# Performance work log

Measured on AMD Instinct MI355X. Metric: run time of the kernel, lower is better.

The kernel has to match this reference:

```python
import jax, jax.numpy as jnp
import numpy as np

B, D, H = 4096, 64, 1024  # batch, state dim, hidden width


def setup_inputs() -> dict:
    key = jax.random.key(0)
    ks = jax.random.split(key, 4)
    def w(k, shape, fan_in):
        return (jax.random.normal(k, shape, jnp.float32) / np.float32(np.sqrt(fan_in)))
    return {
        "x": jax.random.normal(ks[0], (B, 1 + D), jnp.float32),
        "W1": w(ks[1], (D, H), D),
        "b1": jnp.zeros((H,), jnp.float32),
        "W2": w(ks[2], (H, H), H),
        "b2": jnp.zeros((H,), jnp.float32),
        "W3": w(ks[3], (H, D), H),
        "b3": jnp.zeros((D,), jnp.float32),
    }


def _mlp(z, W1, b1, W2, b2, W3, b3):
    # tanh MLP vector field: d -> h -> h -> d
    h = jnp.tanh(z @ W1 + b1)
    h = jnp.tanh(h @ W2 + b2)
    return h @ W3 + b3


def reference(x, W1, b1, W2, b2, W3, b3):
    x_in = x[:, 1:]                        # [B, D] state (col 0 is logp channel)
    f = lambda z: _mlp(z, W1, b1, W2, b2, W3, b3)
    x_out = f(x_in)                        # [B, D]

    # Exact Jacobian trace: same math as the torch per-dim autograd.grad loop,
    # expressed as D forward-mode JVPs vmapped over the identity basis.
    eye = jnp.eye(x_in.shape[1], dtype=x.dtype)

    def diag_entry(e):                     # e: [D] basis vector
        _, t = jax.jvp(f, (x_in,), (jnp.broadcast_to(e, x_in.shape),))
        return t @ e                       # [B] = J[:, i, i]

    trJ = jnp.sum(jax.vmap(diag_entry)(eye), axis=0)  # [B]

    out = jnp.concatenate([-trJ[:, None], x_out], axis=1)  # [B, 1+D]
    return out + 0.0 * x  # faithful to `+ 0 * x` in the original
```

## Files before the change

kernel.cpp:

```cpp
#include <hip/hip_runtime.h>
#include <cmath>

typedef unsigned short u16;
typedef __attribute__((ext_vector_type(8))) short s8v;
typedef __attribute__((ext_vector_type(4))) float f4v;
typedef __attribute__((ext_vector_type(16))) float f16v;

__device__ __forceinline__ u16 f2bf(float f) {
    union { float f; unsigned u; } v; v.f = f;
    unsigned r = v.u + 0x7FFFu + ((v.u >> 16) & 1u);
    return (u16)(r >> 16);
}
__device__ __forceinline__ float tanh_fast(float x) {
    float e = __builtin_amdgcn_exp2f(x * 2.88539008177792681f);
    return 1.f - 2.f * __builtin_amdgcn_rcpf(1.f + e);
}
__device__ __forceinline__ int wslot(int row, int c) {
    return ((((c >> 2) << 6) | ((c & 3) << 4) | (row & 15)) ^ c);
}
__device__ __forceinline__ size_t fragoff(int n, int k) {
    return (((size_t)(n >> 5) * 64 + (k >> 4)) * 64 + (n & 31) + (((k >> 3) & 1) << 5)) * 8 + (k & 7);
}

__launch_bounds__(256)
__global__ void cnf_prep(const float* __restrict__ x, const float* __restrict__ W1,
                         const float* __restrict__ W2, const float* __restrict__ W3,
                         u16* __restrict__ W2Tf, u16* __restrict__ VTf,
                         u16* __restrict__ xb, u16* __restrict__ W1T,
                         u16* __restrict__ W3Tf, float* __restrict__ trJ)
{
    __shared__ float w2s[32][33];
    __shared__ __align__(16) float w1s[64][36];
    const int a = blockIdx.x * 32;
    const int b = blockIdx.y * 32;
    const int t = threadIdx.x;

    #pragma unroll
    for (int it = 0; it < 4; ++it) {
        int idx = t + it * 256;
        w2s[idx >> 5][idx & 31] = W2[(a + (idx >> 5)) * 1024 + b + (idx & 31)];
    }
    #pragma unroll
    for (int it = 0; it < 8; ++it) {
        int idx = t + it * 256;
        w1s[idx >> 5][idx & 31] = W1[(idx >> 5) * 1024 + a + (idx & 31)];
    }
    __syncthreads();

    #pragma unroll
    for (int it = 0; it < 4; ++it) {
        int idx = t + it * 256;
        int rr = idx >> 5, cc = idx & 31;
        W2Tf[fragoff(b + rr, a + cc)] = f2bf(w2s[cc][rr]);
    }
    {
        const int q = t >> 3, pg = t & 7;
        const float* w3row = W3 + (b + q) * 64;
        f4v u = f4v{0.f, 0.f, 0.f, 0.f};
        #pragma unroll
        for (int i4 = 0; i4 < 16; ++i4) {
            f4v w3v = *(const f4v*)&w3row[i4 * 4];
            #pragma unroll
            for (int s = 0; s < 4; ++s) {
                f4v wv = *(const f4v*)&w1s[i4 * 4 + s][pg * 4];
                u += w3v[s] * wv;
            }
        }
        #pragma unroll
        for (int j = 0; j < 4; ++j) {
            const int pp = pg * 4 + j;
            VTf[fragoff(b + q, a + pp)] = f2bf(w2s[pp][q] * u[j]);
        }
    }
    {
        int bid = blockIdx.y * 32 + blockIdx.x;
        int e = bid * 256 + t;
        xb[e] = f2bf(x[(e >> 6) * 65 + 1 + (e & 63)]);
    }
    if (blockIdx.y == 0) {
        int pp = t >> 3, i0 = (t & 7) * 8;
        s8v v;
        #pragma unroll
        for (int j = 0; j < 8; ++j) v[j] = (short)f2bf(w1s[i0 + j][pp]);
        *(s8v*)&W1T[(a + pp) * 64 + i0] = v;
        if (t < 128) trJ[blockIdx.x * 128 + t] = 0.f;
    }
    if (blockIdx.y == 1) {
        int idx = blockIdx.x * 256 + t;
        int n = idx & 63, k0 = (idx >> 6) * 8;
        s8v v;
        #pragma unroll
        for (int j = 0; j < 8; ++j) v[j] = (short)f2bf(W3[(k0 + j) * 64 + n]);
        *(s8v*)&W3Tf[fragoff(n, k0)] = v;
    }
}

__launch_bounds__(256)
__global__ void cnf_gemm1(const u16* __restrict__ xb, const u16* __restrict__ W1T,
                          const float* __restrict__ b1,
                          u16* __restrict__ h1, u16* __restrict__ g1)
{
    __shared__ __align__(16) u16 lds[12 * 1024];
    __shared__ __align__(16) u16 hls[128 * 64];
    __shared__ __align__(16) u16 gls[128 * 64];
    const int t = threadIdx.x;
    const int wave = t >> 6, lane = t & 63;
    const int wm = wave >> 1, wn = wave & 1;
    const int g = lane >> 4, lr = lane & 15;
    const int arow0 = blockIdx.x * 128, bcol0 = blockIdx.y * 64;

    #pragma unroll
    for (int i = 0; i < 4; ++i) {
        int ch = t + i * 256, row = ch >> 3, c = ch & 7;
        *(s8v*)&lds[(row >> 4) * 1024 + wslot(row, c) * 8] =
            *(const s8v*)&xb[(arow0 + row) * 64 + c * 8];
    }
    #pragma unroll
    for (int i = 0; i < 2; ++i) {
        int ch = t + i * 256, row = ch >> 3, c = ch & 7;
        *(s8v*)&lds[(8 + (row >> 4)) * 1024 + wslot(row, c) * 8] =
            *(const s8v*)&W1T[(bcol0 + row) * 64 + c * 8];
    }
    __syncthreads();

    f4v acc[4][2];
    #pragma unroll
    for (int mi = 0; mi < 4; ++mi)
        #pragma unroll
        for (int ni = 0; ni < 2; ++ni) acc[mi][ni] = f4v{0.f,0.f,0.f,0.f};

    #pragma unroll
    for (int ks = 0; ks < 2; ++ks) {
        const int lo = (ks * 64 + (lane ^ ((ks * 4 + g) & 7))) * 8;
        s8v af[4], bf[2];
        #pragma unroll
        for (int mi = 0; mi < 4; ++mi) af[mi] = *(const s8v*)&lds[(wm * 4 + mi) * 1024 + lo];
        #pragma unroll
        for (int ni = 0; ni < 2; ++ni) bf[ni] = *(const s8v*)&lds[(8 + wn * 2 + ni) * 1024 + lo];
        #pragma unroll
        for (int mi = 0; mi < 4; ++mi)
            #pragma unroll
            for (int ni = 0; ni < 2; ++ni)
                acc[mi][ni] = __builtin_amdgcn_mfma_f32_16x16x32_bf16(af[mi], bf[ni], acc[mi][ni], 0, 0, 0);
    }

    #pragma unroll
    for (int mi = 0; mi < 4; ++mi) {
        const int rowl = wm * 64 + mi * 16 + g * 4;
        #pragma unroll
        for (int ni = 0; ni < 2; ++ni) {
            const int coll = wn * 32 + ni * 16 + lr;
            const float bv = b1[bcol0 + coll];
            const int cc = coll >> 3, jj = coll & 7;
            #pragma unroll
            for (int r = 0; r < 4; ++r) {
                const int row = rowl + r;
                float h = tanh_fast(acc[mi][ni][r] + bv);
                int idx = row * 64 + ((cc ^ (row & 7)) << 3) + jj;
                hls[idx] = f2bf(h);
                gls[idx] = f2bf(1.f - h * h);
            }
        }
    }
    __syncthreads();

    #pragma unroll
    for (int i = 0; i < 4; ++i) {
        int id = i * 256 + t;
        int row = id >> 3, ch = id & 7;
        int src = row * 64 + ((ch ^ (row & 7)) << 3);
        size_t dst = (size_t)(arow0 + row) * 1024 + bcol0 + ch * 8;
        *(s8v*)&h1[dst] = *(const s8v*)&hls[src];
        *(s8v*)&g1[dst] = *(const s8v*)&gls[src];
    }
}

#define LOADA(dh, dg, ko) \
    do { dh = *(const s8v*)(h1p + (ko)); dg = *(const s8v*)(g1p + (ko)); } while (0)

#define LOADB(B, kkg)                                                          \
    do { _Pragma("unroll")                                                     \
         for (int _ks = 0; _ks < 2; ++_ks) {                                   \
             size_t _o = (((size_t)(ntb + wn) * 64 + (kkg) * 2 + _ks) * 64 + lane) * 8; \
             B[_ks*2 + 0] = *(const s8v*)&W2Tf[_o];                            \
             B[_ks*2 + 1] = *(const s8v*)&VTf[_o];                             \
         } } while (0)

#define WRITEA(sh, sg, bb)                                                     \
    do { u16* _wb = &lds[bb][0];                                               \
         *(s8v*)&_wb[sdst] = sh; *(s8v*)&_wb[4096 + sdst] = sg; } while (0)

#define MIDBODY(kt, AwH, AwG, AlH, AlG, Bc, Bn)                                \
    {                                                                          \
        if ((kt) < 30) { const int _ko = ((kt) + 2) * 32; LOADA(AlH, AlG, _ko); } \
        if ((kt) < 31) { WRITEA(AwH, AwG, ((kt) + 1) & 1); LOADB(Bn, (kt) + 1); } \
        const u16* buf = &lds[(kt) & 1][0];                                    \
        _Pragma("unroll")                                                      \
        for (int ks = 0; ks < 2; ++ks) {                                       \
            const int lp = (lane ^ ((lane >> 5) << 2) ^ (ks << 1)) * 8;        \
            s8v a1[2], a2[2];                                                  \
            _Pragma("unroll")                                                  \
            for (int mt = 0; mt < 2; ++mt) {                                   \
                const int R = (wrt * 2 + mt) * 2 + ks;                         \
                a1[mt] = *(const s8v*)&buf[R * 512 + lp];                      \
                a2[mt] = *(const s8v*)&buf[4096 + R * 512 + lp];               \
            }                                                                  \
            _Pragma("unroll")                                                  \
            for (int mt = 0; mt < 2; ++mt) {                                   \
                acc1[mt] = __builtin_amdgcn_mfma_f32_32x32x16_bf16(a1[mt], Bc[ks*2+0], acc1[mt], 0, 0, 0); \
                acc2[mt] = __builtin_amdgcn_mfma_f32_32x32x16_bf16(a2[mt], Bc[ks*2+1], acc2[mt], 0, 0, 0); \
            }                                                                  \
        }                                                                      \
        __syncthreads();                                                       \
    }

__launch_bounds__(512, 1)
__global__ void cnf_mid(const u16* __restrict__ h1, const u16* __restrict__ g1,
                        const u16* __restrict__ W2Tf, const u16* __restrict__ VTf,
                        const float* __restrict__ b2,
                        u16* __restrict__ h2f, float* __restrict__ trJ)
{
    __shared__ __align__(16) u16 lds[2][8192];

    const int t = threadIdx.x;
    const int wave = t >> 6, lane = t & 63;
    const int wrt = wave & 1;
    const int wn  = wave >> 1;
    const int arow0 = blockIdx.x * 128;
    const int ntb = blockIdx.y * 4;

    const int row = t >> 2, c = t & 3;
    const int R0 = (row >> 5) * 2 + (c >> 1);
    const int L0 = (row & 31) + ((c & 1) << 5);
    const int sdst = (R0 * 64 + (L0 ^ ((L0 >> 5) << 2) ^ ((R0 & 1) << 1))) * 8;
    const u16* h1p = h1 + (size_t)(arow0 + row) * 1024 + c * 8;
    const u16* g1p = g1 + (size_t)(arow0 + row) * 1024 + c * 8;

    f16v acc1[2], acc2[2];
    #pragma unroll
    for (int mt = 0; mt < 2; ++mt)
        #pragma unroll
        for (int r = 0; r < 16; ++r) { acc1[mt][r] = 0.f; acc2[mt][r] = 0.f; }

    s8v ahA, agA, ahB, agB;
    s8v bA[4], bB[4];

    LOADA(ahA, agA, 0);
    WRITEA(ahA, agA, 0);
    LOADA(ahB, agB, 32);
    LOADB(bA, 0);
    __syncthreads();

    for (int kt2 = 0; kt2 < 16; ++kt2) {
        const int kt = kt2 * 2;
        MIDBODY(kt,     ahB, agB, ahA, agA, bA, bB);
        MIDBODY(kt + 1, ahA, agA, ahB, agB, bB, bA);
    }

    const int l31 = lane & 31, lh = lane >> 5;
    #pragma unroll
    for (int mt = 0; mt < 2; ++mt) {
        const int rt = (arow0 >> 5) + wrt * 2 + mt;
        const int q0 = (ntb + wn) * 32;
        const float bv = b2[q0 + l31];
        const size_t hb = (((size_t)rt * 64 + ((q0 + l31) >> 4)) * 64
                           + (((l31 >> 3) & 1) << 5)) * 8 + (l31 & 7) + lh * 32;
        float tr[16];
        #pragma unroll
        for (int r = 0; r < 16; ++r) {
            float hh = tanh_fast(acc1[mt][r] + bv);
            float gg = 1.f - hh * hh;
            h2f[hb + ((r & 3) + ((r >> 2) << 3)) * 8] = f2bf(hh);
            tr[r] = acc2[mt][r] * gg;
        }
        #pragma unroll
        for (int off = 1; off < 32; off <<= 1)
            #pragma unroll
            for (int r = 0; r < 16; ++r) tr[r] += __shfl_xor(tr[r], off);
        if (l31 == 0) {
            const int rowb = arow0 + (wrt * 2 + mt) * 32 + lh * 4;
            #pragma unroll
            for (int r = 0; r < 16; ++r)
                atomicAdd(&trJ[rowb + (r & 3) + ((r >> 2) << 3)], tr[r]);
        }
    }
}

__launch_bounds__(256)
__global__ void cnf_out(const u16* __restrict__ h2f, const u16* __restrict__ W3Tf,
                        const float* __restrict__ b3, const float* __restrict__ trJ,
                        float* __restrict__ out)
{
    __shared__ float red[4][32][64];
    const int t = threadIdx.x;
    const int wave = t >> 6, lane = t & 63;
    const int rt = blockIdx.x;

    f16v acc[2];
    #pragma unroll
    for (int ni = 0; ni < 2; ++ni)
        #pragma unroll
        for (int r = 0; r < 16; ++r) acc[ni][r] = 0.f;

    #pragma unroll
    for (int kki = 0; kki < 16; ++kki) {
        const int kk = wave * 16 + kki;
        s8v af = *(const s8v*)&h2f[(((size_t)rt * 64 + kk) * 64 + lane) * 8];
        #pragma unroll
        for (int ni = 0; ni < 2; ++ni) {
            s8v bf = *(const s8v*)&W3Tf[(((size_t)ni * 64 + kk) * 64 + lane) * 8];
            acc[ni] = __builtin_amdgcn_mfma_f32_32x32x16_bf16(af, bf, acc[ni], 0, 0, 0);
        }
    }
    const int l31 = lane & 31, lh = lane >> 5;
    #pragma unroll
    for (int ni = 0; ni < 2; ++ni)
        #pragma unroll
        for (int r = 0; r < 16; ++r)
            red[wave][(r & 3) + ((r >> 2) << 3) + lh * 4][ni * 32 + l31] = acc[ni][r];
    __syncthreads();

    #pragma unroll
    for (int i = 0; i < 8; ++i) {
        int o = t * 8 + i;
        int row = o >> 6, col = o & 63;
        float s = red[0][row][col] + red[1][row][col] + red[2][row][col] + red[3][row][col] + b3[col];
        out[(size_t)(rt * 32 + row) * 65 + 1 + col] = s;
    }
    if (t < 32) out[(size_t)(rt * 32 + t) * 65] = -trJ[rt * 32 + t];
}

extern "C" void kernel_launch(void* const* d_in, const int* in_sizes, int n_in,
                              void* d_out, int out_size, void* d_ws, size_t ws_size,
                              hipStream_t stream) {
    const float* x  = (const float*)d_in[0];
    const float* W1 = (const float*)d_in[1];
    const float* b1 = (const float*)d_in[2];
    const float* W2 = (const float*)d_in[3];
    const float* b2 = (const float*)d_in[4];
    const float* W3 = (const float*)d_in[5];
    const float* b3 = (const float*)d_in[6];
    float* out = (float*)d_out;

    char* ws = (char*)d_ws;
    u16*   h1b = (u16*)(ws);
    u16*   g1b = (u16*)(ws + (size_t)( 8u << 20));
    u16*   h2f = (u16*)(ws + (size_t)(16u << 20));
    u16*   W2T = (u16*)(ws + (size_t)(24u << 20));
    u16*   VTb = (u16*)(ws + (size_t)(26u << 20));
    float* trJ = (float*)(ws + (size_t)(28u << 20));
    u16*   xbb = (u16*)(ws + (size_t)(28u << 20) + 65536);
    u16*   W1T = (u16*)(ws + (size_t)(28u << 20) + 65536 + 524288);
    u16*   W3T = (u16*)(ws + (size_t)(28u << 20) + 65536 + 524288 + 131072);

    cnf_prep <<<dim3(32, 32), 256, 0, stream>>>(x, W1, W2, W3, W2T, VTb, xbb, W1T, W3T, trJ);
    cnf_gemm1<<<dim3(32, 16), 256, 0, stream>>>(xbb, W1T, b1, h1b, g1b);
    cnf_mid  <<<dim3(32, 8),  512, 0, stream>>>(h1b, g1b, W2T, VTb, b2, h2f, trJ);
    cnf_out  <<<128,          256, 0, stream>>>(h2f, W3T, b3, trJ, out);
}
```

Baseline: 55.49 us.

## Merge first-layer GEMM into prep kernel and split output GEMM across column halves

The separate gemm1 kernel is folded into the prep launch as extra blockIdx.y rows. Those blocks convert x and W1 to bf16 fragments directly in shared memory, which removes the xb/W1T intermediate buffers and one kernel launch. The output kernel now splits its 64 output columns across two blocks per row tile, doubling the block count to improve occupancy. The cost is a larger shared-memory arena for every prep block, which may lower occupancy of the weight-prep blocks, and some redundant A-fragment loads in the output kernel.

```diff
diff --git a/kernel.cpp b/kernel.cpp
--- a/kernel.cpp
+++ b/kernel.cpp
@@ -25,153 +25,154 @@
 __launch_bounds__(256)
 __global__ void cnf_prep(const float* __restrict__ x, const float* __restrict__ W1,
                          const float* __restrict__ W2, const float* __restrict__ W3,
+                         const float* __restrict__ b1,
                          u16* __restrict__ W2Tf, u16* __restrict__ VTf,
-                         u16* __restrict__ xb, u16* __restrict__ W1T,
-                         u16* __restrict__ W3Tf, float* __restrict__ trJ)
+                         u16* __restrict__ W3Tf,
+                         u16* __restrict__ h1, u16* __restrict__ g1,
+                         float* __restrict__ trJ)
 {
-    __shared__ float w2s[32][33];
-    __shared__ __align__(16) float w1s[64][36];
-    const int a = blockIdx.x * 32;
-    const int b = blockIdx.y * 32;
+    __shared__ __align__(16) char arena[57344];
     const int t = threadIdx.x;
 
-    #pragma unroll
-    for (int it = 0; it < 4; ++it) {
-        int idx = t + it * 256;
-        w2s[idx >> 5][idx & 31] = W2[(a + (idx >> 5)) * 1024 + b + (idx & 31)];
-    }
-    #pragma unroll
-    for (int it = 0; it < 8; ++it) {
-        int idx = t + it * 256;
-        w1s[idx >> 5][idx & 31] = W1[(idx >> 5) * 1024 + a + (idx & 31)];
-    }
-    __syncthreads();
-
-    #pragma unroll
-    for (int it = 0; it < 4; ++it) {
-        int idx = t + it * 256;
-        int rr = idx >> 5, cc = idx & 31;
-        W2Tf[fragoff(b + rr, a + cc)] = f2bf(w2s[cc][rr]);
-    }
-    {
-        const int q = t >> 3, pg = t & 7;
-        const float* w3row = W3 + (b + q) * 64;
-        f4v u = f4v{0.f, 0.f, 0.f, 0.f};
-        #pragma unroll
-        for (int i4 = 0; i4 < 16; ++i4) {
-            f4v w3v = *(const f4v*)&w3row[i4 * 4];
-            #pragma unroll
-            for (int s = 0; s < 4; ++s) {
-                f4v wv = *(const f4v*)&w1s[i4 * 4 + s][pg * 4];
-                u += w3v[s] * wv;
+    if (blockIdx.y < 32) {
+        float (*w2s)[33] = (float (*)[33])arena;
+        float (*w1s)[36] = (float (*)[36])(arena + 4352);
+        const int a = blockIdx.x * 32;
+        const int b = blockIdx.y * 32;
+
+        #pragma unroll
+        for (int it = 0; it < 4; ++it) {
+            int idx = t + it * 256;
+            w2s[idx >> 5][idx & 31] = W2[(a + (idx >> 5)) * 1024 + b + (idx & 31)];
+        }
+        #pragma unroll
+        for (int it = 0; it < 8; ++it) {
+            int idx = t + it * 256;
+            w1s[idx >> 5][idx & 31] = W1[(idx >> 5) * 1024 + a + (idx & 31)];
+        }
+        __syncthreads();
+
+        #pragma unroll
+        for (int it = 0; it < 4; ++it) {
+            int idx = t + it * 256;
+            int rr = idx >> 5, cc = idx & 31;
+            W2Tf[fragoff(b + rr, a + cc)] = f2bf(w2s[cc][rr]);
+        }
+        {
+            const int q = t >> 3, pg = t & 7;
+            const float* w3row = W3 + (b + q) * 64;
+            f4v u = f4v{0.f, 0.f, 0.f, 0.f};
+            #pragma unroll
+            for (int i4 = 0; i4 < 16; ++i4) {
+                f4v w3v = *(const f4v*)&w3row[i4 * 4];
+                #pragma unroll
+                for (int s = 0; s < 4; ++s) {
+                    f4v wv = *(const f4v*)&w1s[i4 * 4 + s][pg * 4];
+                    u += w3v[s] * wv;
+                }
             }
-        }
-        #pragma unroll
-        for (int j = 0; j < 4; ++j) {
-            const int pp = pg * 4 + j;
-            VTf[fragoff(b + q, a + pp)] = f2bf(w2s[pp][q] * u[j]);
-        }
-    }
-    {
-        int bid = blockIdx.y * 32 + blockIdx.x;
-        int e = bid * 256 + t;
-        xb[e] = f2bf(x[(e >> 6) * 65 + 1 + (e & 63)]);
-    }
-    if (blockIdx.y == 0) {
-        int pp = t >> 3, i0 = (t & 7) * 8;
-        s8v v;
-        #pragma unroll
-        for (int j = 0; j < 8; ++j) v[j] = (short)f2bf(w1s[i0 + j][pp]);
-        *(s8v*)&W1T[(a + pp) * 64 + i0] = v;
-        if (t < 128) trJ[blockIdx.x * 128 + t] = 0.f;
-    }
-    if (blockIdx.y == 1) {
-        int idx = blockIdx.x * 256 + t;
-        int n = idx & 63, k0 = (idx >> 6) * 8;
-        s8v v;
-        #pragma unroll
-        for (int j = 0; j < 8; ++j) v[j] = (short)f2bf(W3[(k0 + j) * 64 + n]);
-        *(s8v*)&W3Tf[fragoff(n, k0)] = v;
-    }
-}
-
-__launch_bounds__(256)
-__global__ void cnf_gemm1(const u16* __restrict__ xb, const u16* __restrict__ W1T,
-                          const float* __restrict__ b1,
-                          u16* __restrict__ h1, u16* __restrict__ g1)
-{
-    __shared__ __align__(16) u16 lds[12 * 1024];
-    __shared__ __align__(16) u16 hls[128 * 64];
-    __shared__ __align__(16) u16 gls[128 * 64];
-    const int t = threadIdx.x;
-    const int wave = t >> 6, lane = t & 63;
-    const int wm = wave >> 1, wn = wave & 1;
-    const int g = lane >> 4, lr = lane & 15;
-    const int arow0 = blockIdx.x * 128, bcol0 = blockIdx.y * 64;
-
-    #pragma unroll
-    for (int i = 0; i < 4; ++i) {
-        int ch = t + i * 256, row = ch >> 3, c = ch & 7;
-        *(s8v*)&lds[(row >> 4) * 1024 + wslot(row, c) * 8] =
-            *(const s8v*)&xb[(arow0 + row) * 64 + c * 8];
-    }
-    #pragma unroll
-    for (int i = 0; i < 2; ++i) {
-        int ch = t + i * 256, row = ch >> 3, c = ch & 7;
-        *(s8v*)&lds[(8 + (row >> 4)) * 1024 + wslot(row, c) * 8] =
-            *(const s8v*)&W1T[(bcol0 + row) * 64 + c * 8];
-    }
-    __syncthreads();
-
-    f4v acc[4][2];
-    #pragma unroll
-    for (int mi = 0; mi < 4; ++mi)
-        #pragma unroll
-        for (int ni = 0; ni < 2; ++ni) acc[mi][ni] = f4v{0.f,0.f,0.f,0.f};
-
-    #pragma unroll
-    for (int ks = 0; ks < 2; ++ks) {
-        const int lo = (ks * 64 + (lane ^ ((ks * 4 + g) & 7))) * 8;
-        s8v af[4], bf[2];
-        #pragma unroll
-        for (int mi = 0; mi < 4; ++mi) af[mi] = *(const s8v*)&lds[(wm * 4 + mi) * 1024 + lo];
-        #pragma unroll
-        for (int ni = 0; ni < 2; ++ni) bf[ni] = *(const s8v*)&lds[(8 + wn * 2 + ni) * 1024 + lo];
+            #pragma unroll
+            for (int j = 0; j < 4; ++j) {
+                const int pp = pg * 4 + j;
+                VTf[fragoff(b + q, a + pp)] = f2bf(w2s[pp][q] * u[j]);
+            }
+        }
+        if (blockIdx.y == 0 && t < 128) trJ[blockIdx.x * 128 + t] = 0.f;
+        if (blockIdx.y == 1) {
+            int idx = blockIdx.x * 256 + t;
+            int n = idx & 63, k0 = (idx >> 6) * 8;
+            s8v v;
+            #pragma unroll
+            for (int j = 0; j < 8; ++j) v[j] = (short)f2bf(W3[(k0 + j) * 64 + n]);
+            *(s8v*)&W3Tf[fragoff(n, k0)] = v;
+        }
+    } else {
+        const int wave = t >> 6, lane = t & 63;
+        const int wm = wave >> 1, wn = wave & 1;
+        const int g = lane >> 4, lr = lane & 15;
+        const int arow0 = blockIdx.x * 128;
+        const int bcol0 = (blockIdx.y - 32) * 64;
+
+        u16*  frg = (u16*)arena;
+        float (*w1f)[65] = (float (*)[65])(arena + 24576);
+        u16*  hls = (u16*)(arena + 24576);
+        u16*  gls = (u16*)(arena + 24576 + 16384);
+
+        #pragma unroll
+        for (int it = 0; it < 16; ++it) {
+            int idx = t + it * 256;
+            int row = idx >> 6, col = idx & 63;
+            w1f[row][col] = W1[row * 1024 + bcol0 + col];
+        }
+        #pragma unroll
+        for (int it = 0; it < 32; ++it) {
+            int e = t + it * 256;
+            int row = e >> 6, col = e & 63;
+            frg[(row >> 4) * 1024 + wslot(row, col >> 3) * 8 + (col & 7)] =
+                f2bf(x[(arow0 + row) * 65 + 1 + col]);
+        }
+        __syncthreads();
+        #pragma unroll
+        for (int it = 0; it < 2; ++it) {
+            int id = t + it * 256;
+            int p = id >> 3, c = id & 7;
+            s8v v;
+            #pragma unroll
+            for (int j = 0; j < 8; ++j) v[j] = (short)f2bf(w1f[c * 8 + j][p]);
+            *(s8v*)&frg[(8 + (p >> 4)) * 1024 + wslot(p, c) * 8] = v;
+        }
+        __syncthreads();
+
+        f4v acc[4][2];
         #pragma unroll
         for (int mi = 0; mi < 4; ++mi)
             #pragma unroll
-            for (int ni = 0; ni < 2; ++ni)
-                acc[mi][ni] = __builtin_amdgcn_mfma_f32_16x16x32_bf16(af[mi], bf[ni], acc[mi][ni], 0, 0, 0);
-    }
-
-    #pragma unroll
-    for (int mi = 0; mi < 4; ++mi) {
-        const int rowl = wm * 64 + mi * 16 + g * 4;
-        #pragma unroll
-        for (int ni = 0; ni < 2; ++ni) {
-            const int coll = wn * 32 + ni * 16 + lr;
-            const float bv = b1[bcol0 + coll];
-            const int cc = coll >> 3, jj = coll & 7;
-            #pragma unroll
-            for (int r = 0; r < 4; ++r) {
-                const int row = rowl + r;
-                float h = tanh_fast(acc[mi][ni][r] + bv);
-                int idx = row * 64 + ((cc ^ (row & 7)) << 3) + jj;
-                hls[idx] = f2bf(h);
-                gls[idx] = f2bf(1.f - h * h);
+            for (int ni = 0; ni < 2; ++ni) acc[mi][ni] = f4v{0.f,0.f,0.f,0.f};
+
+        #pragma unroll
+        for (int ks = 0; ks < 2; ++ks) {
+            const int lo = (ks * 64 + (lane ^ ((ks * 4 + g) & 7))) * 8;
+            s8v af[4], bf[2];
+            #pragma unroll
+            for (int mi = 0; mi < 4; ++mi) af[mi] = *(const s8v*)&frg[(wm * 4 + mi) * 1024 + lo];
+            #pragma unroll
+            for (int ni = 0; ni < 2; ++ni) bf[ni] = *(const s8v*)&frg[(8 + wn * 2 + ni) * 1024 + lo];
+            #pragma unroll
+            for (int mi = 0; mi < 4; ++mi)
+                #pragma unroll
+                for (int ni = 0; ni < 2; ++ni)
+                    acc[mi][ni] = __builtin_amdgcn_mfma_f32_16x16x32_bf16(af[mi], bf[ni], acc[mi][ni], 0, 0, 0);
+        }
+
+        #pragma unroll
+        for (int mi = 0; mi < 4; ++mi) {
+            const int rowl = wm * 64 + mi * 16 + g * 4;
+            #pragma unroll
+            for (int ni = 0; ni < 2; ++ni) {
+                const int coll = wn * 32 + ni * 16 + lr;
+                const float bv = b1[bcol0 + coll];
+                const int cc = coll >> 3, jj = coll & 7;
+                #pragma unroll
+                for (int r = 0; r < 4; ++r) {
+                    const int row = rowl + r;
+                    float h = tanh_fast(acc[mi][ni][r] + bv);
+                    int idx = row * 64 + ((cc ^ (row & 7)) << 3) + jj;
+                    hls[idx] = f2bf(h);
+                    gls[idx] = f2bf(1.f - h * h);
+                }
             }
         }
-    }
-    __syncthreads();
-
-    #pragma unroll
-    for (int i = 0; i < 4; ++i) {
-        int id = i * 256 + t;
-        int row = id >> 3, ch = id & 7;
-        int src = row * 64 + ((ch ^ (row & 7)) << 3);
-        size_t dst = (size_t)(arow0 + row) * 1024 + bcol0 + ch * 8;
-        *(s8v*)&h1[dst] = *(const s8v*)&hls[src];
-        *(s8v*)&g1[dst] = *(const s8v*)&gls[src];
+        __syncthreads();
+
+        #pragma unroll
+        for (int i = 0; i < 4; ++i) {
+            int id = i * 256 + t;
+            int row = id >> 3, ch = id & 7;
+            int src = row * 64 + ((ch ^ (row & 7)) << 3);
+            size_t dst = (size_t)(arow0 + row) * 1024 + bcol0 + ch * 8;
+            *(s8v*)&h1[dst] = *(const s8v*)&hls[src];
+            *(s8v*)&g1[dst] = *(const s8v*)&gls[src];
+        }
     }
 }
 
@@ -291,43 +292,38 @@
                         const float* __restrict__ b3, const float* __restrict__ trJ,
                         float* __restrict__ out)
 {
-    __shared__ float red[4][32][64];
+    __shared__ float red[4][32][32];
     const int t = threadIdx.x;
     const int wave = t >> 6, lane = t & 63;
     const int rt = blockIdx.x;
-
-    f16v acc[2];
-    #pragma unroll
-    for (int ni = 0; ni < 2; ++ni)
-        #pragma unroll
-        for (int r = 0; r < 16; ++r) acc[ni][r] = 0.f;
+    const int nb = blockIdx.y;
+
+    f16v acc;
+    #pragma unroll
+    for (int r = 0; r < 16; ++r) acc[r] = 0.f;
 
     #pragma unroll
     for (int kki = 0; kki < 16; ++kki) {
         const int kk = wave * 16 + kki;
         s8v af = *(const s8v*)&h2f[(((size_t)rt * 64 + kk) * 64 + lane) * 8];
-        #pragma unroll
-        for (int ni = 0; ni < 2; ++ni) {
-            s8v bf = *(const s8v*)&W3Tf[(((size_t)ni * 64 + kk) * 64 + lane) * 8];
-            acc[ni] = __builtin_amdgcn_mfma_f32_32x32x16_bf16(af, bf, acc[ni], 0, 0, 0);
-        }
+        s8v bf = *(const s8v*)&W3Tf[(((size_t)nb * 64 + kk) * 64 + lane) * 8];
+        acc = __builtin_amdgcn_mfma_f32_32x32x16_bf16(af, bf, acc, 0, 0, 0);
     }
     const int l31 = lane & 31, lh = lane >> 5;
     #pragma unroll
-    for (int ni = 0; ni < 2; ++ni)
-        #pragma unroll
-        for (int r = 0; r < 16; ++r)
-            red[wave][(r & 3) + ((r >> 2) << 3) + lh * 4][ni * 32 + l31] = acc[ni][r];
+    for (int r = 0; r < 16; ++r)
+        red[wave][(r & 3) + ((r >> 2) << 3) + lh * 4][l31] = acc[r];
     __syncthreads();
 
     #pragma unroll
-    for (int i = 0; i < 8; ++i) {
-        int o = t * 8 + i;
-        int row = o >> 6, col = o & 63;
-        float s = red[0][row][col] + red[1][row][col] + red[2][row][col] + red[3][row][col] + b3[col];
-        out[(size_t)(rt * 32 + row) * 65 + 1 + col] = s;
-    }
-    if (t < 32) out[(size_t)(rt * 32 + t) * 65] = -trJ[rt * 32 + t];
+    for (int i = 0; i < 4; ++i) {
+        int o = t + i * 256;
+        int row = o >> 5, col = o & 31;
+        float s = red[0][row][col] + red[1][row][col] + red[2][row][col]
+                + red[3][row][col] + b3[nb * 32 + col];
+        out[(size_t)(rt * 32 + row) * 65 + 1 + nb * 32 + col] = s;
+    }
+    if (nb == 0 && t < 32) out[(size_t)(rt * 32 + t) * 65] = -trJ[rt * 32 + t];
 }
 
 extern "C" void kernel_launch(void* const* d_in, const int* in_sizes, int n_in,
@@ -349,12 +345,10 @@
     u16*   W2T = (u16*)(ws + (size_t)(24u << 20));
     u16*   VTb = (u16*)(ws + (size_t)(26u << 20));
     float* trJ = (float*)(ws + (size_t)(28u << 20));
-    u16*   xbb = (u16*)(ws + (size_t)(28u << 20) + 65536);
-    u16*   W1T = (u16*)(ws + (size_t)(28u << 20) + 65536 + 524288);
-    u16*   W3T = (u16*)(ws + (size_t)(28u << 20) + 65536 + 524288 + 131072);
-
-    cnf_prep <<<dim3(32, 32), 256, 0, stream>>>(x, W1, W2, W3, W2T, VTb, xbb, W1T, W3T, trJ);
-    cnf_gemm1<<<dim3(32, 16), 256, 0, stream>>>(xbb, W1T, b1, h1b, g1b);
-    cnf_mid  <<<dim3(32, 8),  512, 0, stream>>>(h1b, g1b, W2T, VTb, b2, h2f, trJ);
-    cnf_out  <<<128,          256, 0, stream>>>(h2f, W3T, b3, trJ, out);
-}
+    u16*   W3T = (u16*)(ws + (size_t)(28u << 20) + 65536);
+
+    cnf_prep<<<dim3(32, 48), 256, 0, stream>>>(x, W1, W2, W3, b1,
+                                               W2T, VTb, W3T, h1b, g1b, trJ);
+    cnf_mid <<<dim3(32, 8),  512, 0, stream>>>(h1b, g1b, W2T, VTb, b2, h2f, trJ);
+    cnf_out <<<dim3(128, 2), 256, 0, stream>>>(h2f, W3T, b3, trJ, out);
+}
```

Result: slower. 57.44 us (+3.5%).
